# Kernel tuning notes

Hardware: AMD Instinct MI355X
Metric: run time of the kernel (lower is better)

The kernel has to match this reference:

```python
import jax, jax.numpy as jnp
import numpy as np
from jax import lax

DIM = 256
NUM_HEADS = 8
HEAD_DIM = DIM // NUM_HEADS
SCALE = HEAD_DIM ** -0.5


def _avg_pool(x, k, p):
    # torch AvgPool2d(kernel=k, stride=1, padding=p) with count_include_pad=True
    s = lax.reduce_window(x, 0.0, lax.add,
                          window_dimensions=(1, 1, k, k),
                          window_strides=(1, 1, 1, 1),
                          padding=((0, 0), (0, 0), (p, p), (p, p)))
    return s / (k * k)


def setup_inputs() -> dict:
    key = jax.random.key(0)
    ks = jax.random.split(key, 7)
    x = jax.random.normal(ks[0], (2, DIM, 48, 48), dtype=jnp.float32)
    q_w = jax.random.normal(ks[1], (DIM, DIM), dtype=jnp.float32) * (DIM ** -0.5)
    q_b = jax.random.normal(ks[2], (DIM,), dtype=jnp.float32) * 0.02
    kv_w = jax.random.normal(ks[3], (2 * DIM, DIM), dtype=jnp.float32) * (DIM ** -0.5)
    kv_b = jax.random.normal(ks[4], (2 * DIM,), dtype=jnp.float32) * 0.02
    proj_w = jax.random.normal(ks[5], (DIM, DIM), dtype=jnp.float32) * (DIM ** -0.5)
    proj_b = jax.random.normal(ks[6], (DIM,), dtype=jnp.float32) * 0.02
    return {"x": x, "q_w": q_w, "q_b": q_b, "kv_w": kv_w, "kv_b": kv_b,
            "proj_w": proj_w, "proj_b": proj_b}


def reference(x, q_w, q_b, kv_w, kv_b, proj_w, proj_b):
    B, C, H, W = x.shape
    h, d, N = NUM_HEADS, HEAD_DIM, H * W

    # q = 1x1 conv -> [B, h, N, d]
    q = jnp.einsum('oc,bchw->bohw', q_w, x) + q_b[None, :, None, None]
    q = q.reshape(B, h, d, N).transpose(0, 1, 3, 2)

    # kv is a linear 1x1 conv, so (kv(x)+kv(p1)+kv(p2)+kv(p3))/4 == kv(mean of inputs)
    x_avg = (x + _avg_pool(x, 3, 1) + _avg_pool(x, 5, 2) + _avg_pool(x, 7, 3)) / 4.0
    kv = jnp.einsum('oc,bchw->bohw', kv_w, x_avg) + kv_b[None, :, None, None]
    kv = kv.reshape(B, 2, h, d, N).transpose(1, 0, 2, 4, 3)  # [2, B, h, N, d]
    k, v = kv[0], kv[1]

    attn = jnp.einsum('bhnd,bhmd->bhnm', q, k) * SCALE  # [B, h, N, N]
    attn = jax.nn.softmax(attn, axis=-1)
    y = jnp.einsum('bhnm,bhmd->bhnd', attn, v)  # [B, h, N, d]
    # faithful to torch: transpose(1,2) then flat reshape to [B, C, H, W]
    y = y.transpose(0, 2, 1, 3).reshape(B, C, H, W)

    out = jnp.einsum('oc,bchw->bohw', proj_w, y) + proj_b[None, :, None, None]
    return out
```

## Files before the change

kernel.cpp:

```cpp
#include <hip/hip_runtime.h>
#include <hip/hip_bf16.h>
#include <cstdint>

#define DIMC  256
#define NH    8
#define HD    32
#define NPIX  2304
#define BATCH 2
#define KT    32
#define NWAVE 4
#define NTW   18
#define KPW   576

typedef short s16x8 __attribute__((ext_vector_type(8)));
typedef short s16x4 __attribute__((ext_vector_type(4)));
typedef float f32x4 __attribute__((ext_vector_type(4)));

#define MFMA32(A,B,C) __builtin_amdgcn_mfma_f32_16x16x32_bf16(A,B,C,0,0,0)

__device__ inline uint32_t rnau(float x) { return __float_as_uint(x) + 0x8000u; }
__device__ inline uint32_t pk2(uint32_t l_, uint32_t h_) {
  return __builtin_amdgcn_perm(h_, l_, 0x07060302u);
}

__global__ __launch_bounds__(256) void pool_kernel(const float* __restrict__ x,
                                                   float* __restrict__ xavg) {
  const int plane = blockIdx.x;
  const float* xp = x + (size_t)plane * NPIX;
  __shared__ float sx[NPIX];
  __shared__ float h3[NPIX], h5[NPIX], h7[NPIX];
  const int t = threadIdx.x;
#pragma unroll
  for (int r = 0; r < 9; ++r) sx[r * 256 + t] = xp[r * 256 + t];
  __syncthreads();
#pragma unroll
  for (int r = 0; r < 9; ++r) {
    int p = r * 256 + t;
    int i = p / 48, j = p - i * 48;
    float a3 = 0.f, a5 = 0.f, a7 = 0.f;
#pragma unroll
    for (int dj = -3; dj <= 3; ++dj) {
      int jj = j + dj;
      if (jj < 0 || jj >= 48) continue;
      float v = sx[i * 48 + jj];
      a7 += v;
      if (dj >= -2 && dj <= 2) a5 += v;
      if (dj >= -1 && dj <= 1) a3 += v;
    }
    h3[p] = a3; h5[p] = a5; h7[p] = a7;
  }
  __syncthreads();
#pragma unroll
  for (int r = 0; r < 9; ++r) {
    int p = r * 256 + t;
    int i = p / 48, j = p - i * 48;
    float b3 = 0.f, b5 = 0.f, b7 = 0.f;
#pragma unroll
    for (int di = -3; di <= 3; ++di) {
      int ii = i + di;
      if (ii < 0 || ii >= 48) continue;
      int q = ii * 48 + j;
      b7 += h7[q];
      if (di >= -2 && di <= 2) b5 += h5[q];
      if (di >= -1 && di <= 1) b3 += h3[q];
    }
    xavg[(size_t)plane * NPIX + p] =
        0.25f * (sx[p] + b3 * (1.f / 9.f) + b5 * (1.f / 25.f) + b7 * (1.f / 49.f));
  }
}

__global__ __launch_bounds__(256) void conv_all(
    const float* __restrict__ x, const float* __restrict__ xavg,
    const float* __restrict__ qw, const float* __restrict__ kvw,
    const float* __restrict__ pw_,
    short* __restrict__ Xh, short* __restrict__ Ah,
    short* __restrict__ Wth) {
  const int bx = blockIdx.x;
  const int t = threadIdx.x;
  if (bx < 576) {
    const float* src = (bx < 288) ? x : xavg;
    short* dhi = (bx < 288) ? Xh : Ah;
    const int bb = (bx < 288) ? bx : bx - 288;
    const int n0 = (bb % 36) * 64, c0 = ((bb / 36) & 3) * 64, b = bb / 144;
    __shared__ __align__(16) float T[64][68];
    {
      const int c = t >> 2, n4 = (t & 3) * 16;
      const float* sp = src + ((size_t)b * DIMC + c0 + c) * NPIX + n0 + n4;
#pragma unroll
      for (int i2 = 0; i2 < 4; ++i2)
        *(f32x4*)&T[c][n4 + i2 * 4] = *(const f32x4*)(sp + i2 * 4);
    }
    __syncthreads();
    {
      const int n = t >> 2, c4 = (t & 3) * 16;
      float v[16];
#pragma unroll
      for (int i = 0; i < 16; ++i) v[i] = T[c4 + i][n];
      uint32_t a[16];
#pragma unroll
      for (int i = 0; i < 16; ++i) a[i] = rnau(v[i]);
      union { s16x8 s; uint32_t u[4]; } H0, H1;
#pragma unroll
      for (int j = 0; j < 4; ++j) {
        H0.u[j] = pk2(a[2 * j], a[2 * j + 1]);
        H1.u[j] = pk2(a[8 + 2 * j], a[8 + 2 * j + 1]);
      }
      const size_t off = ((size_t)b * NPIX + n0 + n) * DIMC + c0 + c4;
      *(s16x8*)(dhi + off) = H0.s; *(s16x8*)(dhi + off + 8) = H1.s;
    }
  } else {
    const int idx = ((bx - 576) * 256 + t) * 8;
    const float* s;
    int off;
    if (idx < 65536)       { s = qw;  off = idx; }
    else if (idx < 196608) { s = kvw; off = idx - 65536; }
    else                   { s = pw_; off = idx - 196608; }
    f32x4 x0 = *(const f32x4*)(s + off);
    f32x4 x1 = *(const f32x4*)(s + off + 4);
    float v[8] = {x0[0], x0[1], x0[2], x0[3], x1[0], x1[1], x1[2], x1[3]};
    uint32_t a[8];
#pragma unroll
    for (int i = 0; i < 8; ++i) a[i] = rnau(v[i]);
    union { s16x8 s; uint32_t u[4]; } H;
#pragma unroll
    for (int j = 0; j < 4; ++j) H.u[j] = pk2(a[2 * j], a[2 * j + 1]);
    *(s16x8*)(Wth + idx) = H.s;
  }
}

__global__ __launch_bounds__(128) void gemm_qkv_hi(
    const short* __restrict__ Wth,
    const float* __restrict__ q_b, const float* __restrict__ kv_b,
    const short* __restrict__ Xh, const short* __restrict__ Ah,
    short* __restrict__ Qhi, short* __restrict__ Khi, short* __restrict__ Vhi,
    float qscale) {
  __shared__ __align__(16) float Cl[32][68];
  const int by = blockIdx.y;
  const bool isQ = (by < 8);
  const int o0 = isQ ? by * 32 : (by - 8) * 32;
  const short* Wh = isQ ? Wth : Wth + 65536;
  const float* bias = isQ ? q_b : kv_b;
  const short* Inh = isQ ? Xh : Ah;
  const float scale = isQ ? qscale : 1.0f;
  short* d1 = isQ ? Qhi : Khi;
  const int n0 = blockIdx.x * 64;
  const int b  = blockIdx.z;

  const int tid = threadIdx.x;
  const int wave = tid >> 6, lane = tid & 63;
  const int g = lane >> 4, q = lane & 15;

  const short* wph = Wh + ((o0 + wave * 16 + q) * DIMC + g * 8);
  const short* iph = Inh + ((size_t)(b * NPIX + n0 + q) * DIMC + g * 8);

  f32x4 acc[4] = {{0,0,0,0},{0,0,0,0},{0,0,0,0},{0,0,0,0}};
#pragma unroll
  for (int c0 = 0; c0 < DIMC; c0 += 32) {
    s16x8 ah = *(const s16x8*)(wph + c0);
#pragma unroll
    for (int st = 0; st < 4; ++st) {
      s16x8 bh_ = *(const s16x8*)(iph + (size_t)st * 16 * DIMC + c0);
      acc[st] = MFMA32(ah, bh_, acc[st]);
    }
  }
#pragma unroll
  for (int st = 0; st < 4; ++st)
#pragma unroll
    for (int r = 0; r < 4; ++r)
      Cl[wave * 16 + g * 4 + r][st * 16 + q] = acc[st][r];
  __syncthreads();

  if (o0 < 256) {
    const int n = tid >> 1, oq = tid & 1;
    const int h = o0 >> 5;
    const float* bp = bias + o0 + oq * 16;
    float v[16];
#pragma unroll
    for (int i = 0; i < 16; ++i) v[i] = (Cl[oq * 16 + i][n] + bp[i]) * scale;
    uint32_t a[16];
#pragma unroll
    for (int i = 0; i < 16; ++i) a[i] = rnau(v[i]);
    union { s16x8 s; uint32_t u[4]; } H0, H1;
#pragma unroll
    for (int j = 0; j < 4; ++j) {
      H0.u[j] = pk2(a[2 * j], a[2 * j + 1]);
      H1.u[j] = pk2(a[8 + 2 * j], a[8 + 2 * j + 1]);
    }
    const size_t off = ((size_t)((b * 8 + h) * NPIX + n0 + n)) * HD + oq * 16;
    *(s16x8*)(d1 + off) = H0.s; *(s16x8*)(d1 + off + 8) = H1.s;
  } else {
    const int o = tid >> 2, nc = (tid & 3) * 16;
    const int h = (o0 - 256) >> 5;
    const float bv = bias[o0 + o];
    float v[16];
#pragma unroll
    for (int i2 = 0; i2 < 4; ++i2) {
      f32x4 t4 = *(const f32x4*)&Cl[o][nc + i2 * 4];
      v[i2 * 4 + 0] = t4[0] + bv; v[i2 * 4 + 1] = t4[1] + bv;
      v[i2 * 4 + 2] = t4[2] + bv; v[i2 * 4 + 3] = t4[3] + bv;
    }
    uint32_t a[16];
#pragma unroll
    for (int i = 0; i < 16; ++i) a[i] = rnau(v[i]);
    union { s16x8 s; uint32_t u[4]; } H0, H1;
#pragma unroll
    for (int j = 0; j < 4; ++j) {
      H0.u[j] = pk2(a[2 * j], a[2 * j + 1]);
      H1.u[j] = pk2(a[8 + 2 * j], a[8 + 2 * j + 1]);
    }
    const size_t off = ((size_t)((b * 8 + h) * HD + o)) * NPIX + n0 + nc;
    *(s16x8*)(Vhi + off) = H0.s; *(s16x8*)(Vhi + off + 8) = H1.s;
  }
}

__global__ __launch_bounds__(256) void attn_fused(
    const short* __restrict__ Qhi,
    const short* __restrict__ Khi,
    const short* __restrict__ Vhi,
    short* __restrict__ zh) {
  const int li = blockIdx.x;
  const int r144 = li >> 3;
  const int bh = 2 * (li & 7) + (r144 >= 72 ? 1 : 0);
  const int qb = (r144 >= 72) ? r144 - 72 : r144;
  const int tid = threadIdx.x;
  const int wave = tid >> 6, lane = tid & 63;
  const int g = lane >> 4, q = lane & 15;
  const int base = qb * 32;

  __shared__ __align__(16) float smemf[4 * 64 * 20];
  short* pwA = (short*)smemf + wave * 1280;
  short* pwB = pwA + 640;
  float (*R)[64][20] = (float (*)[64][20])smemf;

  const size_t qoff = ((size_t)bh * NPIX + base + q) * HD + g * 8;
  const s16x8 qhA = *(const s16x8*)(Qhi + qoff);
  const s16x8 qhB = *(const s16x8*)(Qhi + qoff + 16 * HD);

  const short* kp = Khi + ((size_t)bh * NPIX + wave * KPW + q) * HD + g * 8;
  const short* vp = Vhi + ((size_t)bh * HD + q) * NPIX + wave * KPW + g * 8;

  const f32x4 Z4 = {0.f, 0.f, 0.f, 0.f};
  f32x4 OA0 = Z4, OA1 = Z4, OB0 = Z4, OB1 = Z4;
  f32x4 LA = Z4, LB = Z4;
  s16x8 kb[3][2], vb[3][2], pfA, pfB, vp0, vp1;

  union { s16x8 s; uint32_t u[4]; } ONE, ZZ;
  ONE.u[0] = 0x3F803F80u; ONE.u[1] = 0x3F803F80u;
  ONE.u[2] = 0x3F803F80u; ONE.u[3] = 0x3F803F80u;
  ZZ.u[0] = 0; ZZ.u[1] = 0; ZZ.u[2] = 0; ZZ.u[3] = 0;
  const s16x8 ones = ONE.s;
  pfA = ZZ.s; pfB = ZZ.s;
  vp0 = ones; vp1 = ones;

  kb[0][0] = *(const s16x8*)(kp);
  kb[0][1] = *(const s16x8*)(kp + 16 * HD);
  vb[0][0] = *(const s16x8*)(vp);
  vb[0][1] = *(const s16x8*)(vp + 16 * NPIX);
  kb[1][0] = *(const s16x8*)(kp + KT * HD);
  kb[1][1] = *(const s16x8*)(kp + KT * HD + 16 * HD);
  vb[1][0] = *(const s16x8*)(vp + KT);
  vb[1][1] = *(const s16x8*)(vp + KT + 16 * NPIX);

#define ATTN_STEP(CUR, NX2, T)                                                \
  {                                                                           \
    if ((T) + 2 < NTW) {                                                      \
      const short* kpn = kp + ((T) + 2) * (KT * HD);                          \
      const short* vpn = vp + ((T) + 2) * KT;                                 \
      kb[NX2][0] = *(const s16x8*)(kpn);                                      \
      kb[NX2][1] = *(const s16x8*)(kpn + 16 * HD);                            \
      vb[NX2][0] = *(const s16x8*)(vpn);                                      \
      vb[NX2][1] = *(const s16x8*)(vpn + 16 * NPIX);                          \
    }                                                                         \
    f32x4 SA0 = MFMA32(kb[CUR][0], qhA, Z4);                                  \
    f32x4 SA1 = MFMA32(kb[CUR][1], qhA, Z4);                                  \
    f32x4 SB0 = MFMA32(kb[CUR][0], qhB, Z4);                                  \
    f32x4 SB1 = MFMA32(kb[CUR][1], qhB, Z4);                                  \
    OA0 = MFMA32(vp0, pfA, OA0);                                              \
    OA1 = MFMA32(vp1, pfA, OA1);                                              \
    OB0 = MFMA32(vp0, pfB, OB0);                                              \
    OB1 = MFMA32(vp1, pfB, OB1);                                              \
    LA  = MFMA32(ones, pfA, LA);                                              \
    LB  = MFMA32(ones, pfB, LB);                                              \
    {                                                                         \
      f32x4 p0, p1;                                                           \
      p0[0] = exp2f(SA0[0]); p0[1] = exp2f(SA0[1]);                           \
      p0[2] = exp2f(SA0[2]); p0[3] = exp2f(SA0[3]);                           \
      p1[0] = exp2f(SA1[0]); p1[1] = exp2f(SA1[1]);                           \
      p1[2] = exp2f(SA1[2]); p1[3] = exp2f(SA1[3]);                           \
      uint2 w0, w1;                                                           \
      w0.x = pk2(rnau(p0[0]), rnau(p0[1])); w0.y = pk2(rnau(p0[2]), rnau(p0[3])); \
      w1.x = pk2(rnau(p1[0]), rnau(p1[1])); w1.y = pk2(rnau(p1[2]), rnau(p1[3])); \
      *(uint2*)&pwA[q * 40 + g * 4] = w0;                                     \
      *(uint2*)&pwA[q * 40 + 16 + g * 4] = w1;                                \
    }                                                                         \
    {                                                                         \
      f32x4 p0, p1;                                                           \
      p0[0] = exp2f(SB0[0]); p0[1] = exp2f(SB0[1]);                           \
      p0[2] = exp2f(SB0[2]); p0[3] = exp2f(SB0[3]);                           \
      p1[0] = exp2f(SB1[0]); p1[1] = exp2f(SB1[1]);                           \
      p1[2] = exp2f(SB1[2]); p1[3] = exp2f(SB1[3]);                           \
      uint2 w0, w1;                                                           \
      w0.x = pk2(rnau(p0[0]), rnau(p0[1])); w0.y = pk2(rnau(p0[2]), rnau(p0[3])); \
      w1.x = pk2(rnau(p1[0]), rnau(p1[1])); w1.y = pk2(rnau(p1[2]), rnau(p1[3])); \
      *(uint2*)&pwB[q * 40 + g * 4] = w0;                                     \
      *(uint2*)&pwB[q * 40 + 16 + g * 4] = w1;                                \
    }                                                                         \
    vp0 = vb[CUR][0]; vp1 = vb[CUR][1];                                       \
    pfA = *(const s16x8*)&pwA[q * 40 + g * 8];                                \
    pfB = *(const s16x8*)&pwB[q * 40 + g * 8];                                \
  }

#pragma unroll 1
  for (int tt = 0; tt < NTW; tt += 3) {
    ATTN_STEP(0, 2, tt);
    ATTN_STEP(1, 0, tt + 1);
    ATTN_STEP(2, 1, tt + 2);
  }
#undef ATTN_STEP

  OA0 = MFMA32(vp0, pfA, OA0);
  OA1 = MFMA32(vp1, pfA, OA1);
  OB0 = MFMA32(vp0, pfB, OB0);
  OB1 = MFMA32(vp1, pfB, OB1);
  LA  = MFMA32(ones, pfA, LA);
  LB  = MFMA32(ones, pfB, LB);

  __syncthreads();
  {
    float* rw = &R[wave][lane][0];
    *(f32x4*)&rw[0]  = OA0;
    *(f32x4*)&rw[4]  = OA1;
    *(f32x4*)&rw[8]  = OB0;
    *(f32x4*)&rw[12] = OB1;
    rw[16] = LA[0];
    rw[17] = LB[0];
  }
  __syncthreads();
  {
    const int l2 = tid & 63, eg = tid >> 6;
    const int g2 = l2 >> 4, q2 = l2 & 15;
    f32x4 s = {0.f, 0.f, 0.f, 0.f};
    float Lt = 0.f;
#pragma unroll
    for (int w = 0; w < NWAVE; ++w) {
      const f32x4 pv = *(const f32x4*)&R[w][l2][eg * 4];
      s[0] += pv[0]; s[1] += pv[1]; s[2] += pv[2]; s[3] += pv[3];
      Lt += R[w][l2][16 + (eg >> 1)];
    }
    const float inv = 1.f / Lt;
    const int h = bh & 7, b = bh >> 3;
    const int n = base + ((eg & 2) ? 16 : 0) + q2;
    const int d0 = ((eg & 1) ? 16 : 0) + g2 * 4;
    const int c = n / 9, r = n - c * 9;
    short* zp = zh + ((size_t)(b * NPIX + r * 256 + h * HD + d0)) * DIMC + c;
#pragma unroll
    for (int j = 0; j < 4; ++j)
      zp[(size_t)j * DIMC] = (short)(rnau(s[j] * inv) >> 16);
  }
}

__global__ __launch_bounds__(128) void gemm_proj_hi(
    const short* __restrict__ Wh,
    const float* __restrict__ bias,
    const short* __restrict__ Zh,
    float* __restrict__ out) {
  __shared__ __align__(16) float Cl[32][68];
  const int n0 = blockIdx.x * 64;
  const int o0 = blockIdx.y * 32;
  const int b  = blockIdx.z;
  const int tid = threadIdx.x;
  const int wave = tid >> 6, lane = tid & 63;
  const int g = lane >> 4, q = lane & 15;

  const short* wph = Wh + ((o0 + wave * 16 + q) * DIMC + g * 8);
  const short* iph = Zh + ((size_t)(b * NPIX + n0 + q) * DIMC + g * 8);

  f32x4 acc[4] = {{0,0,0,0},{0,0,0,0},{0,0,0,0},{0,0,0,0}};
#pragma unroll
  for (int c0 = 0; c0 < DIMC; c0 += 32) {
    s16x8 ah = *(const s16x8*)(wph + c0);
#pragma unroll
    for (int st = 0; st < 4; ++st) {
      s16x8 bh_ = *(const s16x8*)(iph + (size_t)st * 16 * DIMC + c0);
      acc[st] = MFMA32(ah, bh_, acc[st]);
    }
  }
#pragma unroll
  for (int st = 0; st < 4; ++st)
#pragma unroll
    for (int r = 0; r < 4; ++r)
      Cl[wave * 16 + g * 4 + r][st * 16 + q] = acc[st][r];
  __syncthreads();

  const int o = tid >> 2, nc = (tid & 3) * 16;
  const float bv = bias[o0 + o];
  float* op = out + ((size_t)b * DIMC + o0 + o) * NPIX + n0 + nc;
#pragma unroll
  for (int i2 = 0; i2 < 4; ++i2) {
    f32x4 v = *(const f32x4*)&Cl[o][nc + i2 * 4];
    v[0] += bv; v[1] += bv; v[2] += bv; v[3] += bv;
    *(f32x4*)(op + i2 * 4) = v;
  }
}

extern "C" void kernel_launch(void* const* d_in, const int* in_sizes, int n_in,
                              void* d_out, int out_size, void* d_ws, size_t ws_size,
                              hipStream_t stream) {
  const float* x      = (const float*)d_in[0];
  const float* q_w    = (const float*)d_in[1];
  const float* q_b    = (const float*)d_in[2];
  const float* kv_w   = (const float*)d_in[3];
  const float* kv_b   = (const float*)d_in[4];
  const float* proj_w = (const float*)d_in[5];
  const float* proj_b = (const float*)d_in[6];
  float* out = (float*)d_out;

  char* w = (char*)d_ws;
  float* xavg = (float*)w;
  short* Xh   = (short*)(w + 4718592);
  short* Ah   = (short*)(w + 9437184);
  short* Wth  = (short*)(w + 28311552);
  short* Qhi  = (short*)(w + 29360128);
  short* Khi  = (short*)(w + 31719424);
  short* Vhi  = (short*)(w + 34078720);
  short* Zh   = (short*)(w + 37322752);

  const float qscale = 0.17677669529663689f * 1.4426950408889634f;

  pool_kernel<<<BATCH * DIMC, 256, 0, stream>>>(x, xavg);
  conv_all<<<704, 256, 0, stream>>>(x, xavg, q_w, kv_w, proj_w, Xh, Ah, Wth);
  gemm_qkv_hi<<<dim3(36, 24, 2), 128, 0, stream>>>(Wth, q_b, kv_b,
                                                   Xh, Ah, Qhi, Khi, Vhi, qscale);
  attn_fused<<<1152, 256, 0, stream>>>(Qhi, Khi, Vhi, Zh);
  gemm_proj_hi<<<dim3(36, 8, 2), 128, 0, stream>>>(Wth + 196608, proj_b, Zh, out);
}
```

Measured before the change: 148.7 us.

## Permute V key layout so softmax probabilities feed PV MFMA from registers

```diff
diff --git a/kernel.cpp b/kernel.cpp
--- a/kernel.cpp
+++ b/kernel.cpp
@@ -202,14 +202,15 @@
     uint32_t a[16];
 #pragma unroll
     for (int i = 0; i < 16; ++i) a[i] = rnau(v[i]);
-    union { s16x8 s; uint32_t u[4]; } H0, H1;
+    short* po = Vhi + ((size_t)((b * 8 + h) * HD + o)) * NPIX + n0 + (nc & 32);
+    const int phase = (nc & 16) ? 4 : 0;
 #pragma unroll
     for (int j = 0; j < 4; ++j) {
-      H0.u[j] = pk2(a[2 * j], a[2 * j + 1]);
-      H1.u[j] = pk2(a[8 + 2 * j], a[8 + 2 * j + 1]);
-    }
-    const size_t off = ((size_t)((b * 8 + h) * HD + o)) * NPIX + n0 + nc;
-    *(s16x8*)(Vhi + off) = H0.s; *(s16x8*)(Vhi + off + 8) = H1.s;
+      uint2 wv;
+      wv.x = pk2(a[4 * j], a[4 * j + 1]);
+      wv.y = pk2(a[4 * j + 2], a[4 * j + 3]);
+      *(uint2*)(po + phase + 8 * j) = wv;
+    }
   }
 }
 
@@ -227,10 +228,7 @@
   const int g = lane >> 4, q = lane & 15;
   const int base = qb * 32;
 
-  __shared__ __align__(16) float smemf[4 * 64 * 20];
-  short* pwA = (short*)smemf + wave * 1280;
-  short* pwB = pwA + 640;
-  float (*R)[64][20] = (float (*)[64][20])smemf;
+  __shared__ __align__(16) float R[4][64][20];
 
   const size_t qoff = ((size_t)bh * NPIX + base + q) * HD + g * 8;
   const s16x8 qhA = *(const s16x8*)(Qhi + qoff);
@@ -287,11 +285,12 @@
       p0[2] = exp2f(SA0[2]); p0[3] = exp2f(SA0[3]);                           \
       p1[0] = exp2f(SA1[0]); p1[1] = exp2f(SA1[1]);                           \
       p1[2] = exp2f(SA1[2]); p1[3] = exp2f(SA1[3]);                           \
-      uint2 w0, w1;                                                           \
-      w0.x = pk2(rnau(p0[0]), rnau(p0[1])); w0.y = pk2(rnau(p0[2]), rnau(p0[3])); \
-      w1.x = pk2(rnau(p1[0]), rnau(p1[1])); w1.y = pk2(rnau(p1[2]), rnau(p1[3])); \
-      *(uint2*)&pwA[q * 40 + g * 4] = w0;                                     \
-      *(uint2*)&pwA[q * 40 + 16 + g * 4] = w1;                                \
+      union { s16x8 s; uint32_t u[4]; } PA;                                   \
+      PA.u[0] = pk2(rnau(p0[0]), rnau(p0[1]));                                \
+      PA.u[1] = pk2(rnau(p0[2]), rnau(p0[3]));                                \
+      PA.u[2] = pk2(rnau(p1[0]), rnau(p1[1]));                                \
+      PA.u[3] = pk2(rnau(p1[2]), rnau(p1[3]));                                \
+      pfA = PA.s;                                                             \
     }                                                                         \
     {                                                                         \
       f32x4 p0, p1;                                                           \
@@ -299,15 +298,14 @@
       p0[2] = exp2f(SB0[2]); p0[3] = exp2f(SB0[3]);                           \
       p1[0] = exp2f(SB1[0]); p1[1] = exp2f(SB1[1]);                           \
       p1[2] = exp2f(SB1[2]); p1[3] = exp2f(SB1[3]);                           \
-      uint2 w0, w1;                                                           \
-      w0.x = pk2(rnau(p0[0]), rnau(p0[1])); w0.y = pk2(rnau(p0[2]), rnau(p0[3])); \
-      w1.x = pk2(rnau(p1[0]), rnau(p1[1])); w1.y = pk2(rnau(p1[2]), rnau(p1[3])); \
-      *(uint2*)&pwB[q * 40 + g * 4] = w0;                                     \
-      *(uint2*)&pwB[q * 40 + 16 + g * 4] = w1;                                \
+      union { s16x8 s; uint32_t u[4]; } PB;                                   \
+      PB.u[0] = pk2(rnau(p0[0]), rnau(p0[1]));                                \
+      PB.u[1] = pk2(rnau(p0[2]), rnau(p0[3]));                                \
+      PB.u[2] = pk2(rnau(p1[0]), rnau(p1[1]));                                \
+      PB.u[3] = pk2(rnau(p1[2]), rnau(p1[3]));                                \
+      pfB = PB.s;                                                             \
     }                                                                         \
     vp0 = vb[CUR][0]; vp1 = vb[CUR][1];                                       \
-    pfA = *(const s16x8*)&pwA[q * 40 + g * 8];                                \
-    pfB = *(const s16x8*)&pwB[q * 40 + g * 8];                                \
   }
 
 #pragma unroll 1
@@ -325,7 +323,6 @@
   LA  = MFMA32(ones, pfA, LA);
   LB  = MFMA32(ones, pfB, LB);
 
-  __syncthreads();
   {
     float* rw = &R[wave][lane][0];
     *(f32x4*)&rw[0]  = OA0;
```

New measurement: 147.9 us. Within noise of the previous version (-0.5%).
